# Kernel tuning notes

Hardware: AMD Instinct MI355X
Metric: run time of the kernel (lower is better)

Reference implementation:

```python
import jax, jax.numpy as jnp
import numpy as np

V, E, HT, HC = 30000, 300, 256, 256
B, LC, T = 32, 32, 64
NTAG = 9  # output_dim + 2


def lstm_dir(x, lens, Wih, Whh, b, reverse):
    """Variable-length single-direction LSTM (packed-sequence semantics).
    x: [N, T, D], lens: [N] int. Returns outputs [N, T, H] zeroed at pad steps.
    Masked state update keeps h,c frozen at pad steps, so reverse=True starts
    from each sequence's true last element (zeros carry through leading pads).
    """
    N, Tn, _ = x.shape
    H = Whh.shape[1]
    gx = jnp.einsum('ntd,gd->ntg', x, Wih) + b            # [N,T,4H]
    mask = jnp.arange(Tn)[None, :] < lens[:, None]         # [N,T]

    def step(carry, inp):
        h, c = carry
        g_t, m = inp                                       # [N,4H], [N]
        gates = g_t + h @ Whh.T
        i, f, g, o = jnp.split(gates, 4, axis=-1)
        c_new = jax.nn.sigmoid(f) * c + jax.nn.sigmoid(i) * jnp.tanh(g)
        h_new = jax.nn.sigmoid(o) * jnp.tanh(c_new)
        m = m[:, None]
        h2 = jnp.where(m, h_new, h)
        c2 = jnp.where(m, c_new, c)
        return (h2, c2), jnp.where(m, h2, 0.0)

    init = (jnp.zeros((N, H), x.dtype), jnp.zeros((N, H), x.dtype))
    xs = (jnp.swapaxes(gx, 0, 1), mask.T)
    _, ys = jax.lax.scan(step, init, xs, reverse=reverse)
    return jnp.swapaxes(ys, 0, 1)                          # [N,T,H]


def bilstm(x, lens, Wih_f, Whh_f, b_f, Wih_b, Whh_b, b_b):
    hf = lstm_dir(x, lens, Wih_f, Whh_f, b_f, reverse=False)
    hb = lstm_dir(x, lens, Wih_b, Whh_b, b_b, reverse=True)
    return jnp.concatenate([hf, hb], axis=-1)


def setup_inputs() -> dict:
    key = jax.random.key(0)
    ks = jax.random.split(key, 20)
    s = 0.05
    inp = {
        'x': jax.random.randint(ks[0], (B, LC, T), 0, V, dtype=jnp.int32),
        'x_feats': jax.random.normal(ks[1], (B, LC, 64), jnp.float32),
        'x_len': jnp.maximum(jax.random.randint(ks[2], (B,), 0, LC, dtype=jnp.int32), 1),
        'x_chunk_len': jax.random.randint(ks[3], (B, LC), 1, T + 1, dtype=jnp.int32),
        'emb': jax.random.normal(ks[4], (V, E), jnp.float32) * s,
        'tok_Wih_f': jax.random.normal(ks[5], (4 * HT, E), jnp.float32) * s,
        'tok_Whh_f': jax.random.normal(ks[6], (4 * HT, HT), jnp.float32) * s,
        'tok_b_f': jax.random.normal(ks[7], (4 * HT,), jnp.float32) * s,
        'tok_Wih_b': jax.random.normal(ks[8], (4 * HT, E), jnp.float32) * s,
        'tok_Whh_b': jax.random.normal(ks[9], (4 * HT, HT), jnp.float32) * s,
        'tok_b_b': jax.random.normal(ks[10], (4 * HT,), jnp.float32) * s,
        'chk_Wih_f': jax.random.normal(ks[11], (4 * HC, 2 * HT), jnp.float32) * s,
        'chk_Whh_f': jax.random.normal(ks[12], (4 * HC, HC), jnp.float32) * s,
        'chk_b_f': jax.random.normal(ks[13], (4 * HC,), jnp.float32) * s,
        'chk_Wih_b': jax.random.normal(ks[14], (4 * HC, 2 * HT), jnp.float32) * s,
        'chk_Whh_b': jax.random.normal(ks[15], (4 * HC, HC), jnp.float32) * s,
        'chk_b_b': jax.random.normal(ks[16], (4 * HC,), jnp.float32) * s,
        'fc_W': jax.random.normal(ks[17], (NTAG, 2 * HC), jnp.float32) * s,
        'fc_b': jax.random.normal(ks[18], (NTAG,), jnp.float32) * s,
    }
    return inp


def reference(x, x_feats, x_len, x_chunk_len, emb,
              tok_Wih_f, tok_Whh_f, tok_b_f, tok_Wih_b, tok_Whh_b, tok_b_b,
              chk_Wih_f, chk_Whh_f, chk_b_f, chk_Wih_b, chk_Whh_b, chk_b_b,
              fc_W, fc_b):
    b, lc, t = x.shape
    xe = emb[x].reshape(b * lc, t, -1)                     # [B*LC, T, E]
    clens = jnp.clip(x_chunk_len.reshape(-1), 1, t)        # [B*LC]
    h = bilstm(xe, clens, tok_Wih_f, tok_Whh_f, tok_b_f,
               tok_Wih_b, tok_Whh_b, tok_b_b)              # [B*LC, T, 2HT]
    # gather output at last valid timestep (= [fwd final, bwd one-step])
    last = h[jnp.arange(b * lc), clens - 1]                # [B*LC, 2HT]
    chunks = last.reshape(b, lc, -1)                       # [B, LC, 2HT]
    ch = bilstm(chunks, x_len, chk_Wih_f, chk_Whh_f, chk_b_f,
                chk_Wih_b, chk_Whh_b, chk_b_b)             # [B, LC, 2HC]
    # pad_packed(total_length=LC) gives zeros at pad -> fc sees zeros there
    out = ch @ fc_W.T + fc_b                               # [B, LC, NTAG]
    return out
```

## Files before the change

kernel.cpp:

```cpp
#include <hip/hip_runtime.h>


typedef __attribute__((ext_vector_type(8))) short s16x8;
typedef __attribute__((ext_vector_type(4))) float f32x4;
typedef __attribute__((ext_vector_type(2))) unsigned int u32x2;

__device__ __forceinline__ unsigned short f2bf(float f) {
  unsigned u = __builtin_bit_cast(unsigned, f);
  u += 0x7fff + ((u >> 16) & 1);
  return (unsigned short)(u >> 16);
}
__device__ __forceinline__ float bf2f(unsigned short h) {
  unsigned u = ((unsigned)h) << 16;
  return __builtin_bit_cast(float, u);
}
__device__ __forceinline__ float sigm(float x) { return 1.f / (1.f + __expf(-x)); }
__device__ __forceinline__ float tanh_(float x) { return 1.f - 2.f / (__expf(2.f * x) + 1.f); }

union PK8 { s16x8 v; unsigned short u[8]; };

__global__ void prep_weights(const float* __restrict__ wihf, const float* __restrict__ wihb,
                             const float* __restrict__ wcf, const float* __restrict__ wcb,
                             unsigned short* __restrict__ o_wf, unsigned short* __restrict__ o_wb,
                             unsigned short* __restrict__ o_wcf, unsigned short* __restrict__ o_wcb) {
  const int job = blockIdx.y, r = blockIdx.x, tid = threadIdx.x;
  const float* src; unsigned short* dst; int Ks, Kd;
  switch (job) {
    case 0: src = wihf; dst = o_wf;   Ks = 300; Kd = 320; break;
    case 1: src = wihb; dst = o_wb;   Ks = 300; Kd = 320; break;
    case 2: src = wcf;  dst = o_wcf;  Ks = 512; Kd = 512; break;
    default:src = wcb;  dst = o_wcb;  Ks = 512; Kd = 512; break;
  }
  for (int c = tid; c < Kd; c += 256)
    dst[r * Kd + c] = f2bf(c < Ks ? src[r * Ks + c] : 0.f);
}

__global__ __launch_bounds__(256)
void prep_whh_frag(const float* __restrict__ w0, const float* __restrict__ w1,
                   const float* __restrict__ w2,
                   unsigned short* __restrict__ o0, unsigned short* __restrict__ o1,
                   unsigned short* __restrict__ o2) {
  const float* src = blockIdx.y == 0 ? w0 : (blockIdx.y == 1 ? w1 : w2);
  unsigned short* dst = blockIdx.y == 0 ? o0 : (blockIdx.y == 1 ? o1 : o2);
  const int fid = blockIdx.x;
  const int b = fid & 1, g = (fid >> 1) & 3, kt = (fid >> 3) & 7, js = fid >> 6;
  for (int i = threadIdx.x; i < 512; i += 256) {
    const int lane = i >> 3, e = i & 7;
    const int cc = lane & 15, qq = lane >> 4;
    const int row = g * 256 + (js * 2 + b) * 16 + cc;
    const int col = kt * 32 + qq * 8 + e;
    dst[(size_t)fid * 512 + i] = f2bf(src[row * 256 + col]);
  }
}

__global__ void prep_small(const int* __restrict__ x, const int* __restrict__ xcl,
                           int* __restrict__ clens, int* __restrict__ lastv,
                           int* __restrict__ order, int* __restrict__ glen) {
  __shared__ int start[65];
  const int n = threadIdx.x;
  if (n < 65) start[n] = 0;
  __syncthreads();
  int len = xcl[n]; len = len < 1 ? 1 : (len > 64 ? 64 : len);
  clens[n] = len;
  lastv[n] = x[n * 64 + len - 1];
  atomicAdd(&start[len], 1);
  __syncthreads();
  if (n == 0) {
    int acc = 0;
    for (int l = 64; l >= 1; --l) { int h = start[l]; start[l] = acc; acc += h; }
  }
  __syncthreads();
  int pos = atomicAdd(&start[len], 1);
  order[pos] = n;
  __syncthreads();
  if (n < 64) glen[n] = clens[order[n * 16]];
}

__global__ __launch_bounds__(256, 2)
void gemm_bf(const float* __restrict__ A, const int* __restrict__ rowmap,
             int Mrows, int Astride, int Klog, int KP,
             const unsigned short* __restrict__ B, unsigned short* __restrict__ C) {
  __shared__ unsigned short As[128 * 40];
  __shared__ unsigned short Ep[4][64 * 136];
  const int tid = threadIdx.x;
  const int lane = tid & 63, w = tid >> 6;
  const int wrow = w >> 1, wcol = w & 1;
  const int cc = lane & 15, qq = lane >> 4;
  const int m0 = blockIdx.y * 128, n0 = blockIdx.x * 256;

  f32x4 zz = {0.f, 0.f, 0.f, 0.f};
  f32x4 acc[4][8];
#pragma unroll
  for (int i = 0; i < 4; ++i)
#pragma unroll
    for (int j = 0; j < 8; ++j) acc[i][j] = zz;

  const int arow = tid >> 1, ahalf = tid & 1;
  const float* arp = nullptr;
  {
    int av = m0 + arow;
    if (av < Mrows) {
      int amap = rowmap ? rowmap[av] : av;
      arp = A + (long)amap * Astride;
    }
  }

  const int nktiles = KP >> 5;
  for (int kt = 0; kt < nktiles; ++kt) {
    const int k0 = kt << 5;
    __syncthreads();
    {
      const int kb = k0 + ahalf * 16;
      unsigned short hv[16];
      if (arp && kb + 16 <= Klog) {
        const float* p = arp + kb;
#pragma unroll
        for (int i = 0; i < 16; i += 4) {
          f32x4 t = *(const f32x4*)(p + i);
          hv[i] = f2bf(t.x); hv[i + 1] = f2bf(t.y);
          hv[i + 2] = f2bf(t.z); hv[i + 3] = f2bf(t.w);
        }
      } else {
#pragma unroll
        for (int i = 0; i < 16; ++i) {
          float v = (arp && (kb + i) < Klog) ? arp[kb + i] : 0.f;
          hv[i] = f2bf(v);
        }
      }
      PK8 p0, p1;
#pragma unroll
      for (int i = 0; i < 8; ++i) { p0.u[i] = hv[i]; p1.u[i] = hv[8 + i]; }
      *(s16x8*)&As[arow * 40 + ahalf * 16] = p0.v;
      *(s16x8*)&As[arow * 40 + ahalf * 16 + 8] = p1.v;
    }
    __syncthreads();
    s16x8 af[4];
#pragma unroll
    for (int mt = 0; mt < 4; ++mt)
      af[mt] = *(const s16x8*)&As[(wrow * 64 + mt * 16 + cc) * 40 + qq * 8];
#pragma unroll
    for (int nt = 0; nt < 8; ++nt) {
      const unsigned short* bp = B + (long)(n0 + wcol * 128 + nt * 16 + cc) * KP + k0 + qq * 8;
      s16x8 bfr = *(const s16x8*)bp;
#pragma unroll
      for (int mt = 0; mt < 4; ++mt)
        acc[mt][nt] = __builtin_amdgcn_mfma_f32_16x16x32_bf16(af[mt], bfr, acc[mt][nt], 0, 0, 0);
    }
  }
  __syncthreads();
#pragma unroll
  for (int mt = 0; mt < 4; ++mt)
#pragma unroll
    for (int nt = 0; nt < 8; ++nt)
#pragma unroll
      for (int r = 0; r < 4; ++r)
        Ep[w][(mt * 16 + qq * 4 + r) * 136 + nt * 16 + cc] = f2bf(acc[mt][nt][r]);
  __syncthreads();
#pragma unroll
  for (int it = 0; it < 16; ++it) {
    int row = it * 4 + qq;
    s16x8 d = *(const s16x8*)&Ep[w][row * 136 + cc * 8];
    int gm = m0 + wrow * 64 + row;
    int gn = n0 + wcol * 128 + cc * 8;
    if (gm < Mrows) *(s16x8*)&C[(long)gm * 1024 + gn] = d;
  }
}

__global__ void bwd_step(const unsigned short* __restrict__ gxb,
                         const float* __restrict__ bias,
                         float* __restrict__ chunks) {
  const int n = blockIdx.x, j = threadIdx.x;
  const unsigned short* row = gxb + (long)n * 1024;
  float gi = bf2f(row[j]) + bias[j];
  float gg = bf2f(row[512 + j]) + bias[512 + j];
  float go = bf2f(row[768 + j]) + bias[768 + j];
  float cn = sigm(gi) * tanh_(gg);
  chunks[(long)n * 512 + 256 + j] = sigm(go) * tanh_(cn);
}

__global__ __launch_bounds__(256)
void gather_gx(const unsigned short* __restrict__ proj, const int* __restrict__ x,
               const int* __restrict__ order, const int* __restrict__ clens,
               const int* __restrict__ glen, const float* __restrict__ bias,
               unsigned short* __restrict__ gx) {
  const int t = blockIdx.x, p = blockIdx.y, j = threadIdx.x;
  if (t >= glen[p >> 4]) return;
  const int seq = order[p];
  const int len = clens[seq];
  unsigned short* dst = gx + (((size_t)(p >> 4) * 64 + t) * 16 + (p & 15)) * 1024 + j * 4;
  if (t >= len) { u32x2 z = {0u, 0u}; *(u32x2*)dst = z; return; }
  const int tok = x[seq * 64 + t];
  const unsigned short* src = proj + (size_t)tok * 1024 + j;
  unsigned v0 = f2bf(bf2f(src[0]) + bias[j]);
  unsigned v1 = f2bf(bf2f(src[256]) + bias[256 + j]);
  unsigned v2 = f2bf(bf2f(src[512]) + bias[512 + j]);
  unsigned v3 = f2bf(bf2f(src[768]) + bias[768 + j]);
  u32x2 pk = {v0 | (v1 << 16), v2 | (v3 << 16)};
  *(u32x2*)dst = pk;
}

__global__ __launch_bounds__(256)
void repack4(const unsigned short* __restrict__ s0, const unsigned short* __restrict__ s1,
             const float* __restrict__ b0, const float* __restrict__ b1,
             unsigned short* __restrict__ d0, unsigned short* __restrict__ d1) {
  const int r = blockIdx.x, j = threadIdx.x;
  const int m = r >> 5, t = r & 31;
  const int mg = m >> 4, m16 = m & 15;
  const unsigned short* s = (blockIdx.y ? s1 : s0) + (size_t)r * 1024;
  const float* bb = blockIdx.y ? b1 : b0;
  unsigned short* d = (blockIdx.y ? d1 : d0) +
                      (size_t)((mg * 32 + t) * 16 + m16) * 1024 + j * 4;
  unsigned v0 = f2bf(bf2f(s[j]) + bb[j]);
  unsigned v1 = f2bf(bf2f(s[256 + j]) + bb[256 + j]);
  unsigned v2 = f2bf(bf2f(s[512 + j]) + bb[512 + j]);
  unsigned v3 = f2bf(bf2f(s[768 + j]) + bb[768 + j]);
  u32x2 pk = {v0 | (v1 << 16), v2 | (v3 << 16)};
  *(u32x2*)d = pk;
}

__global__ __launch_bounds__(1024, 4)
void tok_fwd(const unsigned short* __restrict__ gx,
             const unsigned short* __restrict__ WhP,
             const int* __restrict__ order,
             const int* __restrict__ clens,
             const int* __restrict__ glen,
             float* __restrict__ chunks) {
  extern __shared__ unsigned short smem[];
  unsigned short* hly = smem;
  unsigned short* ldsW = smem + 4224;
  int* sg = (int*)(smem + 69760);
  int* slen = sg + 16;

  const int tid = threadIdx.x;
  const int lane = tid & 63, w = tid >> 6;
  const int cc = lane & 15, qq = lane >> 4;
  const int gb = blockIdx.x;

  if (tid < 16) {
    int s = order[gb * 16 + tid];
    sg[tid] = s;
    slen[tid] = clens[s];
  }
  for (int i = tid; i < 4224; i += 1024) hly[i] = 0;

  const unsigned short* wgl = WhP + ((size_t)(w >> 1) * 64 + (w & 1)) * 512 + lane * 8;
  {
    unsigned short* ld = ldsW + w * 4096 + lane * 8;
#pragma unroll
    for (int kt = 0; kt < 2; ++kt)
#pragma unroll
      for (int g = 0; g < 4; ++g)
        *(s16x8*)&ld[(kt * 4 + g) * 512] = *(const s16x8*)&wgl[(kt * 8 + g * 2) * 512];
  }
  s16x8 Rw[4];
#pragma unroll
  for (int g = 0; g < 4; ++g) Rw[g] = *(const s16x8*)&wgl[(16 + g * 2) * 512];

  __syncthreads();

  const int maxlen = glen[gb];
  const int j = w * 16 + cc;
  int lenr[4];
#pragma unroll
  for (int r = 0; r < 4; ++r) lenr[r] = slen[qq * 4 + r];

  float cst[4];
#pragma unroll
  for (int r = 0; r < 4; ++r) cst[r] = 0.f;

  const unsigned short* gx0 = gx + (size_t)gb * 64 * 16 * 1024 + j * 4;
  const unsigned short* ldw = ldsW + w * 4096 + lane * 8;
  f32x4 zz = {0.f, 0.f, 0.f, 0.f};

  for (int t = 0; t < maxlen; ++t) {
    __syncthreads();

    u32x2 gxp[4];
#pragma unroll
    for (int r = 0; r < 4; ++r) {
      const int m = qq * 4 + r;
      gxp[r] = *(const u32x2*)(gx0 + ((size_t)t * 16 + m) * 1024);
    }

    f32x4 acc[4];
#pragma unroll
    for (int g = 0; g < 4; ++g) acc[g] = zz;

#pragma unroll
    for (int kt = 0; kt < 2; ++kt) {
      s16x8 a0 = *(const s16x8*)&hly[cc * 264 + kt * 32 + qq * 8];
#pragma unroll
      for (int g = 0; g < 4; ++g) {
        s16x8 bf = *(const s16x8*)&ldw[(kt * 4 + g) * 512];
        acc[g] = __builtin_amdgcn_mfma_f32_16x16x32_bf16(a0, bf, acc[g], 0, 0, 0);
      }
    }
    {
      s16x8 a0 = *(const s16x8*)&hly[cc * 264 + 2 * 32 + qq * 8];
#pragma unroll
      for (int g = 0; g < 4; ++g)
        acc[g] = __builtin_amdgcn_mfma_f32_16x16x32_bf16(a0, Rw[g], acc[g], 0, 0, 0);
    }
#pragma unroll 1
    for (int kt = 3; kt < 8; ++kt) {
      s16x8 Sb[4];
#pragma unroll
      for (int g = 0; g < 4; ++g)
        Sb[g] = *(const s16x8*)&wgl[(kt * 8 + g * 2) * 512];
      s16x8 a0 = *(const s16x8*)&hly[cc * 264 + kt * 32 + qq * 8];
#pragma unroll
      for (int g = 0; g < 4; ++g)
        acc[g] = __builtin_amdgcn_mfma_f32_16x16x32_bf16(a0, Sb[g], acc[g], 0, 0, 0);
    }

    __syncthreads();

#pragma unroll
    for (int r = 0; r < 4; ++r) {
      const int m = qq * 4 + r;
      const u32x2 pk = gxp[r];
      float gi = acc[0][r] + bf2f((unsigned short)(pk.x & 0xffff));
      float gf = acc[1][r] + bf2f((unsigned short)(pk.x >> 16));
      float gg = acc[2][r] + bf2f((unsigned short)(pk.y & 0xffff));
      float go = acc[3][r] + bf2f((unsigned short)(pk.y >> 16));
      if (t < lenr[r]) {
        float cn = sigm(gf) * cst[r] + sigm(gi) * tanh_(gg);
        cst[r] = cn;
        float hn = sigm(go) * tanh_(cn);
        hly[m * 264 + j] = f2bf(hn);
      }
    }
  }

  __syncthreads();
#pragma unroll
  for (int r = 0; r < 4; ++r) {
    const int m = qq * 4 + r;
    chunks[(size_t)sg[m] * 512 + j] = bf2f(hly[m * 264 + j]);
  }
}

__global__ __launch_bounds__(1024, 4)
void chunk_rec(const unsigned short* __restrict__ gxf,
               const unsigned short* __restrict__ gxb,
               const unsigned short* __restrict__ WhPf,
               const unsigned short* __restrict__ WhPb,
               const int* __restrict__ xlen,
               unsigned short* __restrict__ ch) {
  extern __shared__ unsigned short smem[];
  unsigned short* hly = smem;
  unsigned short* ldsW = smem + 4224;

  const int tid = threadIdx.x;
  const int lane = tid & 63, w = tid >> 6;
  const int cc = lane & 15, qq = lane >> 4;
  const int dir = blockIdx.x & 1, mg = blockIdx.x >> 1;
  const unsigned short* gx = (dir ? gxb : gxf) + (size_t)mg * 32 * 16 * 1024;
  const unsigned short* WhP = dir ? WhPb : WhPf;

  for (int i = tid; i < 4224; i += 1024) hly[i] = 0;

  const unsigned short* wgl = WhP + ((size_t)(w >> 1) * 64 + (w & 1)) * 512 + lane * 8;
  {
    unsigned short* ld = ldsW + w * 4096 + lane * 8;
#pragma unroll
    for (int kt = 0; kt < 2; ++kt)
#pragma unroll
      for (int g = 0; g < 4; ++g)
        *(s16x8*)&ld[(kt * 4 + g) * 512] = *(const s16x8*)&wgl[(kt * 8 + g * 2) * 512];
  }
  s16x8 Rw[4];
#pragma unroll
  for (int g = 0; g < 4; ++g) Rw[g] = *(const s16x8*)&wgl[(16 + g * 2) * 512];

  __syncthreads();

  const int j = w * 16 + cc;
  int lenr[4];
#pragma unroll
  for (int r = 0; r < 4; ++r) {
    int L = xlen[mg * 16 + qq * 4 + r];
    lenr[r] = L > 32 ? 32 : L;
  }

  float cst[4];
#pragma unroll
  for (int r = 0; r < 4; ++r) cst[r] = 0.f;

  const unsigned short* ldw = ldsW + w * 4096 + lane * 8;
  f32x4 zz = {0.f, 0.f, 0.f, 0.f};

  for (int tt = 0; tt < 32; ++tt) {
    const int t = dir ? (31 - tt) : tt;

    __syncthreads();

    u32x2 gxp[4];
#pragma unroll
    for (int r = 0; r < 4; ++r) {
      const int m = qq * 4 + r;
      gxp[r] = *(const u32x2*)(gx + ((size_t)t * 16 + m) * 1024 + j * 4);
    }

    f32x4 acc[4];
#pragma unroll
    for (int g = 0; g < 4; ++g) acc[g] = zz;

#pragma unroll
    for (int kt = 0; kt < 2; ++kt) {
      s16x8 a0 = *(const s16x8*)&hly[cc * 264 + kt * 32 + qq * 8];
#pragma unroll
      for (int g = 0; g < 4; ++g) {
        s16x8 bf = *(const s16x8*)&ldw[(kt * 4 + g) * 512];
        acc[g] = __builtin_amdgcn_mfma_f32_16x16x32_bf16(a0, bf, acc[g], 0, 0, 0);
      }
    }
    {
      s16x8 a0 = *(const s16x8*)&hly[cc * 264 + 2 * 32 + qq * 8];
#pragma unroll
      for (int g = 0; g < 4; ++g)
        acc[g] = __builtin_amdgcn_mfma_f32_16x16x32_bf16(a0, Rw[g], acc[g], 0, 0, 0);
    }
#pragma unroll 1
    for (int kt = 3; kt < 8; ++kt) {
      s16x8 Sb[4];
#pragma unroll
      for (int g = 0; g < 4; ++g)
        Sb[g] = *(const s16x8*)&wgl[(kt * 8 + g * 2) * 512];
      s16x8 a0 = *(const s16x8*)&hly[cc * 264 + kt * 32 + qq * 8];
#pragma unroll
      for (int g = 0; g < 4; ++g)
        acc[g] = __builtin_amdgcn_mfma_f32_16x16x32_bf16(a0, Sb[g], acc[g], 0, 0, 0);
    }

    __syncthreads();

#pragma unroll
    for (int r = 0; r < 4; ++r) {
      const int m = qq * 4 + r;
      const u32x2 pk = gxp[r];
      float gi = acc[0][r] + bf2f((unsigned short)(pk.x & 0xffff));
      float gf = acc[1][r] + bf2f((unsigned short)(pk.x >> 16));
      float gg = acc[2][r] + bf2f((unsigned short)(pk.y & 0xffff));
      float go = acc[3][r] + bf2f((unsigned short)(pk.y >> 16));
      unsigned short hb16 = 0;
      if (t < lenr[r]) {
        float cn = sigm(gf) * cst[r] + sigm(gi) * tanh_(gg);
        cst[r] = cn;
        float hn = sigm(go) * tanh_(cn);
        hb16 = f2bf(hn);
        hly[m * 264 + j] = hb16;
      }
      ch[(size_t)((mg * 16 + m) * 32 + t) * 512 + dir * 256 + j] = hb16;
    }
  }
}

__global__ __launch_bounds__(64)
void fc_kernel(const unsigned short* __restrict__ ch, const float* __restrict__ W,
               const float* __restrict__ bfc, float* __restrict__ out) {
  const int n = blockIdx.x, lane = threadIdx.x;
  float xv[8];
  const unsigned short* cp = ch + (long)n * 512 + lane * 8;
#pragma unroll
  for (int i = 0; i < 8; ++i) xv[i] = bf2f(cp[i]);
  float s[9];
#pragma unroll
  for (int k = 0; k < 9; ++k) {
    const float* wr = W + k * 512 + lane * 8;
    float t = 0.f;
#pragma unroll
    for (int i = 0; i < 8; ++i) t += xv[i] * wr[i];
    s[k] = t;
  }
#pragma unroll
  for (int off = 32; off; off >>= 1)
#pragma unroll
    for (int k = 0; k < 9; ++k) s[k] += __shfl_down(s[k], off, 64);
  if (lane == 0) {
#pragma unroll
    for (int k = 0; k < 9; ++k) out[n * 9 + k] = s[k] + bfc[k];
  }
}

extern "C" void kernel_launch(void* const* d_in, const int* in_sizes, int n_in,
                              void* d_out, int out_size, void* d_ws, size_t ws_size,
                              hipStream_t stream) {
  const int*   x           = (const int*)d_in[0];
  const int*   x_len       = (const int*)d_in[2];
  const int*   x_chunk_len = (const int*)d_in[3];
  const float* emb         = (const float*)d_in[4];
  const float* tok_Wih_f   = (const float*)d_in[5];
  const float* tok_Whh_f   = (const float*)d_in[6];
  const float* tok_b_f     = (const float*)d_in[7];
  const float* tok_Wih_b   = (const float*)d_in[8];
  const float* tok_b_b     = (const float*)d_in[10];
  const float* chk_Wih_f   = (const float*)d_in[11];
  const float* chk_Whh_f   = (const float*)d_in[12];
  const float* chk_b_f     = (const float*)d_in[13];
  const float* chk_Wih_b   = (const float*)d_in[14];
  const float* chk_Whh_b   = (const float*)d_in[15];
  const float* chk_b_b     = (const float*)d_in[16];
  const float* fc_W        = (const float*)d_in[17];
  const float* fc_b        = (const float*)d_in[18];
  float* out = (float*)d_out;

  char* ws = (char*)d_ws;
  size_t off = 0;
  auto alloc = [&](size_t bytes) -> void* {
    void* p = ws + off;
    off += (bytes + 255) & ~(size_t)255;
    return p;
  };
  unsigned short* Wf   = (unsigned short*)alloc((size_t)1024 * 320 * 2);
  unsigned short* Wb   = (unsigned short*)alloc((size_t)1024 * 320 * 2);
  unsigned short* Wcf  = (unsigned short*)alloc((size_t)1024 * 512 * 2);
  unsigned short* Wcb  = (unsigned short*)alloc((size_t)1024 * 512 * 2);
  unsigned short* WhPtok=(unsigned short*)alloc((size_t)512 * 512 * 2);
  unsigned short* WhPcf= (unsigned short*)alloc((size_t)512 * 512 * 2);
  unsigned short* WhPcb= (unsigned short*)alloc((size_t)512 * 512 * 2);
  unsigned short* proj = (unsigned short*)alloc((size_t)30000 * 1024 * 2);
  unsigned short* gxbb = (unsigned short*)alloc((size_t)1024 * 1024 * 2);
  unsigned short* gxcf = (unsigned short*)alloc((size_t)1024 * 1024 * 2);
  unsigned short* gxcb = (unsigned short*)alloc((size_t)1024 * 1024 * 2);
  unsigned short* gxcfp= (unsigned short*)alloc((size_t)1024 * 1024 * 2);
  unsigned short* gxcbp= (unsigned short*)alloc((size_t)1024 * 1024 * 2);
  float*          chunks = (float*)alloc((size_t)1024 * 512 * 4);
  unsigned short* cho  = (unsigned short*)alloc((size_t)1024 * 512 * 2);
  unsigned short* gxs  = (unsigned short*)alloc((size_t)1024 * 64 * 1024 * 2);
  int* clens = (int*)alloc(1024 * 4);
  int* lastv = (int*)alloc(1024 * 4);
  int* order = (int*)alloc(1024 * 4);
  int* glen  = (int*)alloc(64 * 4);

  hipFuncSetAttribute((const void*)tok_fwd,
                      hipFuncAttributeMaxDynamicSharedMemorySize, 139776);
  hipFuncSetAttribute((const void*)chunk_rec,
                      hipFuncAttributeMaxDynamicSharedMemorySize, 139520);

  prep_weights<<<dim3(1024, 4), 256, 0, stream>>>(
      tok_Wih_f, tok_Wih_b, chk_Wih_f, chk_Wih_b, Wf, Wb, Wcf, Wcb);
  prep_whh_frag<<<dim3(512, 3), 256, 0, stream>>>(
      tok_Whh_f, chk_Whh_f, chk_Whh_b, WhPtok, WhPcf, WhPcb);
  prep_small<<<1, 1024, 0, stream>>>(x, x_chunk_len, clens, lastv, order, glen);

  gemm_bf<<<dim3(4, 235), 256, 0, stream>>>(emb, nullptr, 30000, 300, 300, 320, Wf, proj);
  gemm_bf<<<dim3(4, 8), 256, 0, stream>>>(emb, lastv, 1024, 300, 300, 320, Wb, gxbb);
  bwd_step<<<1024, 256, 0, stream>>>(gxbb, tok_b_b, chunks);
  gather_gx<<<dim3(64, 1024), 256, 0, stream>>>(proj, x, order, clens, glen, tok_b_f, gxs);
  tok_fwd<<<64, 1024, 139776, stream>>>(gxs, WhPtok, order, clens, glen, chunks);
  gemm_bf<<<dim3(4, 8), 256, 0, stream>>>(chunks, nullptr, 1024, 512, 512, 512, Wcf, gxcf);
  gemm_bf<<<dim3(4, 8), 256, 0, stream>>>(chunks, nullptr, 1024, 512, 512, 512, Wcb, gxcb);
  repack4<<<dim3(1024, 2), 256, 0, stream>>>(gxcf, gxcb, chk_b_f, chk_b_b, gxcfp, gxcbp);
  chunk_rec<<<4, 1024, 139520, stream>>>(gxcfp, gxcbp, WhPcf, WhPcb, x_len, cho);
  fc_kernel<<<1024, 64, 0, stream>>>(cho, fc_W, fc_b, out);
}
```

Baseline: 911.2 us.

## Double-buffer LSTM hidden state and keep recurrent weights in registers

Both recurrent kernels now ping-pong the hidden state between two LDS buffers, which removes the second barrier in each timestep. Recurrent weight fragments for k-tiles 2-7 are held in 24 VGPR vectors instead of being reloaded from global memory every step. Masked rows carry their frozen h in a register so it can be written to the new buffer. The gather kernel no longer writes zeros for padded steps, because the recurrence ignores them. The risk is much higher register pressure at 1024 threads, which could cause spills, plus extra LDS.

After: 883.6 us. -3.0%, faster.

```diff
diff --git a/kernel.cpp b/kernel.cpp
--- a/kernel.cpp
+++ b/kernel.cpp
@@ -187,8 +187,8 @@
   if (t >= glen[p >> 4]) return;
   const int seq = order[p];
   const int len = clens[seq];
+  if (t >= len) return;
   unsigned short* dst = gx + (((size_t)(p >> 4) * 64 + t) * 16 + (p & 15)) * 1024 + j * 4;
-  if (t >= len) { u32x2 z = {0u, 0u}; *(u32x2*)dst = z; return; }
   const int tok = x[seq * 64 + t];
   const unsigned short* src = proj + (size_t)tok * 1024 + j;
   unsigned v0 = f2bf(bf2f(src[0]) + bias[j]);
@@ -226,9 +226,9 @@
              const int* __restrict__ glen,
              float* __restrict__ chunks) {
   extern __shared__ unsigned short smem[];
-  unsigned short* hly = smem;
-  unsigned short* ldsW = smem + 4224;
-  int* sg = (int*)(smem + 69760);
+  unsigned short* hbuf = smem;
+  unsigned short* ldsW = smem + 8448;
+  int* sg = (int*)(smem + 8448 + 65536);
   int* slen = sg + 16;
 
   const int tid = threadIdx.x;
@@ -241,7 +241,7 @@
     sg[tid] = s;
     slen[tid] = clens[s];
   }
-  for (int i = tid; i < 4224; i += 1024) hly[i] = 0;
+  for (int i = tid; i < 4224; i += 1024) hbuf[i] = 0;
 
   const unsigned short* wgl = WhP + ((size_t)(w >> 1) * 64 + (w & 1)) * 512 + lane * 8;
   {
@@ -252,9 +252,12 @@
       for (int g = 0; g < 4; ++g)
         *(s16x8*)&ld[(kt * 4 + g) * 512] = *(const s16x8*)&wgl[(kt * 8 + g * 2) * 512];
   }
-  s16x8 Rw[4];
-#pragma unroll
-  for (int g = 0; g < 4; ++g) Rw[g] = *(const s16x8*)&wgl[(16 + g * 2) * 512];
+  s16x8 Rw[24];
+#pragma unroll
+  for (int kt = 2; kt < 8; ++kt)
+#pragma unroll
+    for (int g = 0; g < 4; ++g)
+      Rw[(kt - 2) * 4 + g] = *(const s16x8*)&wgl[(kt * 8 + g * 2) * 512];
 
   __syncthreads();
 
@@ -265,22 +268,24 @@
   for (int r = 0; r < 4; ++r) lenr[r] = slen[qq * 4 + r];
 
   float cst[4];
-#pragma unroll
-  for (int r = 0; r < 4; ++r) cst[r] = 0.f;
+  unsigned short hreg[4];
+#pragma unroll
+  for (int r = 0; r < 4; ++r) { cst[r] = 0.f; hreg[r] = 0; }
 
   const unsigned short* gx0 = gx + (size_t)gb * 64 * 16 * 1024 + j * 4;
   const unsigned short* ldw = ldsW + w * 4096 + lane * 8;
   f32x4 zz = {0.f, 0.f, 0.f, 0.f};
 
   for (int t = 0; t < maxlen; ++t) {
+    const unsigned short* hr = hbuf + (t & 1) * 4224;
+    unsigned short* hw = hbuf + ((t & 1) ^ 1) * 4224;
+
     __syncthreads();
 
     u32x2 gxp[4];
 #pragma unroll
-    for (int r = 0; r < 4; ++r) {
-      const int m = qq * 4 + r;
-      gxp[r] = *(const u32x2*)(gx0 + ((size_t)t * 16 + m) * 1024);
-    }
+    for (int r = 0; r < 4; ++r)
+      gxp[r] = *(const u32x2*)(gx0 + ((size_t)t * 16 + qq * 4 + r) * 1024);
 
     f32x4 acc[4];
 #pragma unroll
@@ -288,32 +293,20 @@
 
 #pragma unroll
     for (int kt = 0; kt < 2; ++kt) {
-      s16x8 a0 = *(const s16x8*)&hly[cc * 264 + kt * 32 + qq * 8];
+      s16x8 a0 = *(const s16x8*)&hr[cc * 264 + kt * 32 + qq * 8];
 #pragma unroll
       for (int g = 0; g < 4; ++g) {
         s16x8 bf = *(const s16x8*)&ldw[(kt * 4 + g) * 512];
         acc[g] = __builtin_amdgcn_mfma_f32_16x16x32_bf16(a0, bf, acc[g], 0, 0, 0);
       }
     }
-    {
-      s16x8 a0 = *(const s16x8*)&hly[cc * 264 + 2 * 32 + qq * 8];
+#pragma unroll
+    for (int kt = 2; kt < 8; ++kt) {
+      s16x8 a0 = *(const s16x8*)&hr[cc * 264 + kt * 32 + qq * 8];
 #pragma unroll
       for (int g = 0; g < 4; ++g)
-        acc[g] = __builtin_amdgcn_mfma_f32_16x16x32_bf16(a0, Rw[g], acc[g], 0, 0, 0);
-    }
-#pragma unroll 1
-    for (int kt = 3; kt < 8; ++kt) {
-      s16x8 Sb[4];
-#pragma unroll
-      for (int g = 0; g < 4; ++g)
-        Sb[g] = *(const s16x8*)&wgl[(kt * 8 + g * 2) * 512];
-      s16x8 a0 = *(const s16x8*)&hly[cc * 264 + kt * 32 + qq * 8];
-#pragma unroll
-      for (int g = 0; g < 4; ++g)
-        acc[g] = __builtin_amdgcn_mfma_f32_16x16x32_bf16(a0, Sb[g], acc[g], 0, 0, 0);
-    }
-
-    __syncthreads();
+        acc[g] = __builtin_amdgcn_mfma_f32_16x16x32_bf16(a0, Rw[(kt - 2) * 4 + g], acc[g], 0, 0, 0);
+    }
 
 #pragma unroll
     for (int r = 0; r < 4; ++r) {
@@ -326,18 +319,15 @@
       if (t < lenr[r]) {
         float cn = sigm(gf) * cst[r] + sigm(gi) * tanh_(gg);
         cst[r] = cn;
-        float hn = sigm(go) * tanh_(cn);
-        hly[m * 264 + j] = f2bf(hn);
+        hreg[r] = f2bf(sigm(go) * tanh_(cn));
       }
-    }
-  }
-
-  __syncthreads();
-#pragma unroll
-  for (int r = 0; r < 4; ++r) {
-    const int m = qq * 4 + r;
-    chunks[(size_t)sg[m] * 512 + j] = bf2f(hly[m * 264 + j]);
-  }
+      hw[m * 264 + j] = hreg[r];
+    }
+  }
+
+#pragma unroll
+  for (int r = 0; r < 4; ++r)
+    chunks[(size_t)sg[qq * 4 + r] * 512 + j] = bf2f(hreg[r]);
 }
 
 __global__ __launch_bounds__(1024, 4)
@@ -348,8 +338,8 @@
                const int* __restrict__ xlen,
                unsigned short* __restrict__ ch) {
   extern __shared__ unsigned short smem[];
-  unsigned short* hly = smem;
-  unsigned short* ldsW = smem + 4224;
+  unsigned short* hbuf = smem;
+  unsigned short* ldsW = smem + 8448;
 
   const int tid = threadIdx.x;
   const int lane = tid & 63, w = tid >> 6;
@@ -358,7 +348,7 @@
   const unsigned short* gx = (dir ? gxb : gxf) + (size_t)mg * 32 * 16 * 1024;
   const unsigned short* WhP = dir ? WhPb : WhPf;
 
-  for (int i = tid; i < 4224; i += 1024) hly[i] = 0;
+  for (int i = tid; i < 4224; i += 1024) hbuf[i] = 0;
 
   const unsigned short* wgl = WhP + ((size_t)(w >> 1) * 64 + (w & 1)) * 512 + lane * 8;
   {
@@ -369,9 +359,12 @@
       for (int g = 0; g < 4; ++g)
         *(s16x8*)&ld[(kt * 4 + g) * 512] = *(const s16x8*)&wgl[(kt * 8 + g * 2) * 512];
   }
-  s16x8 Rw[4];
-#pragma unroll
-  for (int g = 0; g < 4; ++g) Rw[g] = *(const s16x8*)&wgl[(16 + g * 2) * 512];
+  s16x8 Rw[24];
+#pragma unroll
+  for (int kt = 2; kt < 8; ++kt)
+#pragma unroll
+    for (int g = 0; g < 4; ++g)
+      Rw[(kt - 2) * 4 + g] = *(const s16x8*)&wgl[(kt * 8 + g * 2) * 512];
 
   __syncthreads();
 
@@ -384,23 +377,24 @@
   }
 
   float cst[4];
-#pragma unroll
-  for (int r = 0; r < 4; ++r) cst[r] = 0.f;
+  unsigned short hreg[4];
+#pragma unroll
+  for (int r = 0; r < 4; ++r) { cst[r] = 0.f; hreg[r] = 0; }
 
   const unsigned short* ldw = ldsW + w * 4096 + lane * 8;
   f32x4 zz = {0.f, 0.f, 0.f, 0.f};
 
   for (int tt = 0; tt < 32; ++tt) {
     const int t = dir ? (31 - tt) : tt;
+    const unsigned short* hr = hbuf + (tt & 1) * 4224;
+    unsigned short* hw = hbuf + ((tt & 1) ^ 1) * 4224;
 
     __syncthreads();
 
     u32x2 gxp[4];
 #pragma unroll
-    for (int r = 0; r < 4; ++r) {
-      const int m = qq * 4 + r;
-      gxp[r] = *(const u32x2*)(gx + ((size_t)t * 16 + m) * 1024 + j * 4);
-    }
+    for (int r = 0; r < 4; ++r)
+      gxp[r] = *(const u32x2*)(gx + ((size_t)t * 16 + qq * 4 + r) * 1024 + j * 4);
 
     f32x4 acc[4];
 #pragma unroll
@@ -408,32 +402,20 @@
 
 #pragma unroll
     for (int kt = 0; kt < 2; ++kt) {
-      s16x8 a0 = *(const s16x8*)&hly[cc * 264 + kt * 32 + qq * 8];
+      s16x8 a0 = *(const s16x8*)&hr[cc * 264 + kt * 32 + qq * 8];
 #pragma unroll
       for (int g = 0; g < 4; ++g) {
         s16x8 bf = *(const s16x8*)&ldw[(kt * 4 + g) * 512];
         acc[g] = __builtin_amdgcn_mfma_f32_16x16x32_bf16(a0, bf, acc[g], 0, 0, 0);
       }
     }
-    {
-      s16x8 a0 = *(const s16x8*)&hly[cc * 264 + 2 * 32 + qq * 8];
+#pragma unroll
+    for (int kt = 2; kt < 8; ++kt) {
+      s16x8 a0 = *(const s16x8*)&hr[cc * 264 + kt * 32 + qq * 8];
 #pragma unroll
       for (int g = 0; g < 4; ++g)
-        acc[g] = __builtin_amdgcn_mfma_f32_16x16x32_bf16(a0, Rw[g], acc[g], 0, 0, 0);
-    }
-#pragma unroll 1
-    for (int kt = 3; kt < 8; ++kt) {
-      s16x8 Sb[4];
-#pragma unroll
-      for (int g = 0; g < 4; ++g)
-        Sb[g] = *(const s16x8*)&wgl[(kt * 8 + g * 2) * 512];
-      s16x8 a0 = *(const s16x8*)&hly[cc * 264 + kt * 32 + qq * 8];
-#pragma unroll
-      for (int g = 0; g < 4; ++g)
-        acc[g] = __builtin_amdgcn_mfma_f32_16x16x32_bf16(a0, Sb[g], acc[g], 0, 0, 0);
-    }
-
-    __syncthreads();
+        acc[g] = __builtin_amdgcn_mfma_f32_16x16x32_bf16(a0, Rw[(kt - 2) * 4 + g], acc[g], 0, 0, 0);
+    }
 
 #pragma unroll
     for (int r = 0; r < 4; ++r) {
@@ -443,15 +425,15 @@
       float gf = acc[1][r] + bf2f((unsigned short)(pk.x >> 16));
       float gg = acc[2][r] + bf2f((unsigned short)(pk.y & 0xffff));
       float go = acc[3][r] + bf2f((unsigned short)(pk.y >> 16));
-      unsigned short hb16 = 0;
+      unsigned short out16 = 0;
       if (t < lenr[r]) {
         float cn = sigm(gf) * cst[r] + sigm(gi) * tanh_(gg);
         cst[r] = cn;
-        float hn = sigm(go) * tanh_(cn);
-        hb16 = f2bf(hn);
-        hly[m * 264 + j] = hb16;
+        hreg[r] = f2bf(sigm(go) * tanh_(cn));
+        out16 = hreg[r];
       }
-      ch[(size_t)((mg * 16 + m) * 32 + t) * 512 + dir * 256 + j] = hb16;
+      hw[m * 264 + j] = hreg[r];
+      ch[(size_t)((mg * 16 + m) * 32 + t) * 512 + dir * 256 + j] = out16;
     }
   }
 }
@@ -534,9 +516,9 @@
   int* glen  = (int*)alloc(64 * 4);
 
   hipFuncSetAttribute((const void*)tok_fwd,
-                      hipFuncAttributeMaxDynamicSharedMemorySize, 139776);
+                      hipFuncAttributeMaxDynamicSharedMemorySize, 148096);
   hipFuncSetAttribute((const void*)chunk_rec,
-                      hipFuncAttributeMaxDynamicSharedMemorySize, 139520);
+                      hipFuncAttributeMaxDynamicSharedMemorySize, 147968);
 
   prep_weights<<<dim3(1024, 4), 256, 0, stream>>>(
       tok_Wih_f, tok_Wih_b, chk_Wih_f, chk_Wih_b, Wf, Wb, Wcf, Wcb);
@@ -548,10 +530,10 @@
   gemm_bf<<<dim3(4, 8), 256, 0, stream>>>(emb, lastv, 1024, 300, 300, 320, Wb, gxbb);
   bwd_step<<<1024, 256, 0, stream>>>(gxbb, tok_b_b, chunks);
   gather_gx<<<dim3(64, 1024), 256, 0, stream>>>(proj, x, order, clens, glen, tok_b_f, gxs);
-  tok_fwd<<<64, 1024, 139776, stream>>>(gxs, WhPtok, order, clens, glen, chunks);
+  tok_fwd<<<64, 1024, 148096, stream>>>(gxs, WhPtok, order, clens, glen, chunks);
   gemm_bf<<<dim3(4, 8), 256, 0, stream>>>(chunks, nullptr, 1024, 512, 512, 512, Wcf, gxcf);
   gemm_bf<<<dim3(4, 8), 256, 0, stream>>>(chunks, nullptr, 1024, 512, 512, 512, Wcb, gxcb);
   repack4<<<dim3(1024, 2), 256, 0, stream>>>(gxcf, gxcb, chk_b_f, chk_b_b, gxcfp, gxcbp);
-  chunk_rec<<<4, 1024, 139520, stream>>>(gxcfp, gxcbp, WhPcf, WhPcb, x_len, cho);
+  chunk_rec<<<4, 1024, 147968, stream>>>(gxcfp, gxcbp, WhPcf, WhPcb, x_len, cho);
   fc_kernel<<<1024, 64, 0, stream>>>(cho, fc_W, fc_b, out);
 }
```
